# Kernel tuning notes

Measured on AMD Instinct MI355X. Metric: run time of the kernel, lower is better.

The kernel has to match this reference:

```python
import jax, jax.numpy as jnp
import numpy as np

B, S, H = 1, 2048, 2048
NH, NKV, HD = 16, 4, 128
F, E, TOPK = 4096, 8, 2
EPS = 1e-5
THETA = 10000.0
NEG = -1e30


def setup_inputs() -> dict:
    key = jax.random.key(0)
    ks = jax.random.split(key, 12)
    s = 0.02
    f32 = jnp.float32
    return {
        "positions": jnp.arange(S, dtype=jnp.int32),
        "hidden_states": jax.random.normal(ks[0], (B, S, H), f32),
        "wq": jax.random.normal(ks[1], (H, NH * HD), f32) * s,
        "wk": jax.random.normal(ks[2], (H, NKV * HD), f32) * s,
        "wv": jax.random.normal(ks[3], (H, NKV * HD), f32) * s,
        "wo": jax.random.normal(ks[4], (NH * HD, H), f32) * s,
        "w_gate": jax.random.normal(ks[5], (H, E), f32) * s,
        "w1": jax.random.normal(ks[6], (E, H, F), f32) * s,
        "w2": jax.random.normal(ks[7], (E, F, H), f32) * s,
        "w3": jax.random.normal(ks[8], (E, H, F), f32) * s,
        "ln_in": jnp.ones((H,), f32),
        "ln_post": jnp.ones((H,), f32),
    }


def rmsnorm(x, w):
    var = jnp.mean(jnp.square(x.astype(jnp.float32)), axis=-1, keepdims=True)
    return (x.astype(jnp.float32) * jax.lax.rsqrt(var + EPS)).astype(x.dtype) * w


def apply_rope(x, positions):
    # x: [B, S, n, HD], neox style (rotate halves)
    half = HD // 2
    inv_freq = 1.0 / (THETA ** (jnp.arange(half, dtype=jnp.float32) * 2.0 / HD))
    ang = positions.astype(jnp.float32)[:, None] * inv_freq  # [S, half]
    cos = jnp.cos(ang)[None, :, None, :]
    sin = jnp.sin(ang)[None, :, None, :]
    x1, x2 = jnp.split(x, 2, axis=-1)
    return jnp.concatenate([x1 * cos - x2 * sin, x2 * cos + x1 * sin], axis=-1).astype(x.dtype)


def decoder_layer(positions, x, wq, wk, wv, wo, w_gate, w1, w2, w3, ln_in, ln_post):
    # residual is None branch: residual = x; h = input_layernorm(x)
    residual = x
    h = rmsnorm(x, ln_in)
    # --- attention ---
    q = (h @ wq).reshape(B, S, NH, HD)
    k = (h @ wk).reshape(B, S, NKV, HD)
    v = (h @ wv).reshape(B, S, NKV, HD)
    q = apply_rope(q, positions)
    k = apply_rope(k, positions)
    rep = NH // NKV  # GQA: repeat kv heads
    k = jnp.repeat(k, rep, axis=2)
    v = jnp.repeat(v, rep, axis=2)
    scores = jnp.einsum("bqhd,bkhd->bhqk", q, k) * (HD ** -0.5)
    causal = jnp.tril(jnp.ones((S, S), bool))
    scores = jnp.where(causal[None, None], scores, NEG)
    attn = jax.nn.softmax(scores, axis=-1)
    o = jnp.einsum("bhqk,bkhd->bqhd", attn, v).reshape(B, S, NH * HD) @ wo
    # --- fused add + post-attention RMSNorm ---
    residual = o + residual
    h = rmsnorm(residual, ln_post)
    # --- MoE: dense all-expert compute, mask-weighted combine ---
    xt = h.reshape(-1, H)  # [T, H]
    logits = xt @ w_gate
    rw = jax.nn.softmax(logits.astype(jnp.float32), axis=-1)  # [T, E]
    w_top, idx = jax.lax.top_k(rw, TOPK)
    w_top = w_top / jnp.sum(w_top, axis=-1, keepdims=True)
    T = xt.shape[0]
    combine = jnp.zeros((T, E), jnp.float32).at[jnp.arange(T)[:, None], idx].add(w_top)
    a = jnp.einsum("th,ehf->etf", xt, w1)  # [E, T, F]
    g = jax.nn.silu(a) * jnp.einsum("th,ehf->etf", xt, w3)
    out = jnp.einsum("etf,efh->eth", g, w2)  # [E, T, H]
    moe = jnp.einsum("eth,te->th", out, combine.astype(xt.dtype))
    return moe.reshape(B, S, H), residual


def reference(positions, hidden_states, wq, wk, wv, wo, w_gate, w1, w2, w3, ln_in, ln_post):
    return decoder_layer(positions, hidden_states, wq, wk, wv, wo, w_gate, w1, w2, w3, ln_in, ln_post)
```

## Files before the change

kernel.cpp:

```cpp
#include <hip/hip_runtime.h>

typedef _Float16 f16x8 __attribute__((ext_vector_type(8)));
typedef _Float16 f16x2 __attribute__((ext_vector_type(2)));
typedef float f32x4 __attribute__((ext_vector_type(4)));

#define DEV __device__ __forceinline__

struct alignas(16) H8 { _Float16 h[8]; };
struct alignas(8)  H4 { _Float16 h[4]; };

DEV f32x4 mfma16(f16x8 a, f16x8 b, f32x4 c) {
  return __builtin_amdgcn_mfma_f32_16x16x32_f16(a, b, c, 0, 0, 0);
}

DEV f16x2 pkrtz(float a, float b) {
  return __builtin_bit_cast(f16x2, __builtin_amdgcn_cvt_pkrtz(a, b));
}

DEV H4 pack4(float a, float b, float c, float d) {
  union { f16x2 v[2]; H4 h; } u;
  u.v[0] = pkrtz(a, b);
  u.v[1] = pkrtz(c, d);
  return u.h;
}

DEV f16x8 frag_b36(const _Float16* b, int n, int kc) {
  const unsigned long long* p = (const unsigned long long*)(b + n*36 + kc*8);
  union { unsigned long long u[2]; f16x8 v; } r;
  r.u[0] = p[0]; r.u[1] = p[1];
  return r.v;
}

DEV float block_sum(float v, volatile float* red, int tid) {
  #pragma unroll
  for (int mm = 1; mm < 64; mm <<= 1) v += __shfl_xor(v, mm);
  if ((tid & 63) == 0) red[tid >> 6] = v;
  __syncthreads();
  return red[0] + red[1] + red[2] + red[3];
}

__global__ __launch_bounds__(256) void k_rmsnorm_split(
    const float* __restrict__ x, const float* __restrict__ w,
    _Float16* __restrict__ hi, _Float16* __restrict__ lo) {
  __shared__ float red[4];
  int row = blockIdx.x, tid = threadIdx.x;
  const float* xr = x + (size_t)row*2048 + tid*8;
  float xs[8];
  *(float4*)&xs[0] = *(const float4*)xr;
  *(float4*)&xs[4] = *(const float4*)(xr + 4);
  float ss = 0.f;
  #pragma unroll
  for (int j = 0; j < 8; ++j) ss += xs[j]*xs[j];
  float tot = block_sum(ss, red, tid);
  float sc = 1.0f / sqrtf(tot*(1.0f/2048.0f) + 1e-5f);
  const float* wr = w + tid*8;
  H8 ph, pl;
  #pragma unroll
  for (int j = 0; j < 8; ++j) {
    float o = xs[j]*sc*wr[j];
    _Float16 hh = (_Float16)o;
    ph.h[j] = hh; pl.h[j] = (_Float16)(o - (float)hh);
  }
  *(H8*)(hi + (size_t)row*2048 + tid*8) = ph;
  *(H8*)(lo + (size_t)row*2048 + tid*8) = pl;
}

template<bool RESID>
__global__ __launch_bounds__(256) void k_gemm(
    const _Float16* __restrict__ Ahi, const _Float16* __restrict__ Alo,
    const float* __restrict__ B, int N, int K,
    float* __restrict__ C,
    const float* __restrict__ resid_in, float* __restrict__ resid_out) {
  const int tid = threadIdx.x;
  const int l = tid & 63, w = tid >> 6;
  const int wm = w >> 1, wn = w & 1;
  const int row0 = blockIdx.y * 128, col0 = blockIdx.x * 128;

  __shared__ _Float16 aHi[128*32], aLo[128*32];
  __shared__ _Float16 bHi[128*36], bLo[128*36];

  f32x4 acc[4][4] = {};

  const int rS = tid >> 1, khalf = tid & 1;
  const int bn = tid & 127, bkg = tid >> 7;

  for (int k0 = 0; k0 < K; k0 += 32) {
    __syncthreads();
    {
      int c0 = khalf*2;
      int d0 = rS*32 + ((c0    ) ^ (rS&3))*8;
      int d1 = rS*32 + ((c0 + 1) ^ (rS&3))*8;
      const _Float16* ah = Ahi + (size_t)(row0 + rS)*K + k0 + khalf*16;
      const _Float16* al = Alo + (size_t)(row0 + rS)*K + k0 + khalf*16;
      *(H8*)&aHi[d0] = *(const H8*)ah;
      *(H8*)&aHi[d1] = *(const H8*)(ah + 8);
      *(H8*)&aLo[d0] = *(const H8*)al;
      *(H8*)&aLo[d1] = *(const H8*)(al + 8);
    }
    {
      const float* bp = B + (size_t)(k0 + bkg*16)*N + col0 + bn;
      float tv[16];
      #pragma unroll
      for (int i = 0; i < 16; ++i) tv[i] = bp[(size_t)i*N];
      #pragma unroll
      for (int q_ = 0; q_ < 4; ++q_) {
        H4 ph, pl;
        #pragma unroll
        for (int j = 0; j < 4; ++j) {
          float x = tv[q_*4 + j];
          _Float16 hh = (_Float16)x;
          ph.h[j] = hh; pl.h[j] = (_Float16)(x - (float)hh);
        }
        int ei = bn*36 + bkg*16 + q_*4;
        *(H4*)&bHi[ei] = ph;
        *(H4*)&bLo[ei] = pl;
      }
    }
    __syncthreads();
    {
      const int kc = l >> 4;
      f16x8 ah[4], al4[4];
      #pragma unroll
      for (int m = 0; m < 4; ++m) {
        int mr = wm*64 + m*16 + (l & 15);
        int cc = (kc ^ (mr & 3))*8;
        ah[m]  = *(const f16x8*)&aHi[mr*32 + cc];
        al4[m] = *(const f16x8*)&aLo[mr*32 + cc];
      }
      #pragma unroll
      for (int n = 0; n < 4; ++n) {
        int nr = wn*64 + n*16 + (l & 15);
        f16x8 bh = frag_b36(bHi, nr, kc);
        f16x8 bl = frag_b36(bLo, nr, kc);
        #pragma unroll
        for (int m = 0; m < 4; ++m) {
          acc[m][n] = mfma16(ah[m],  bh, acc[m][n]);
          acc[m][n] = mfma16(ah[m],  bl, acc[m][n]);
          acc[m][n] = mfma16(al4[m], bh, acc[m][n]);
        }
      }
    }
  }
  #pragma unroll
  for (int m = 0; m < 4; ++m)
    #pragma unroll
    for (int n = 0; n < 4; ++n)
      #pragma unroll
      for (int r = 0; r < 4; ++r) {
        int row = row0 + wm*64 + m*16 + (l>>4)*4 + r;
        int col = col0 + wn*64 + n*16 + (l&15);
        float v = acc[m][n][r];
        if constexpr (RESID) {
          size_t idx = (size_t)row*2048 + col;
          v += resid_in[idx];
          resid_out[idx] = v;
        } else {
          C[(size_t)row*N + col] = v;
        }
      }
}

__global__ __launch_bounds__(256) void k_rope(
    float* __restrict__ buf, const int* __restrict__ pos, int nh) {
  int s = blockIdx.x;
  int hh = blockIdx.y*4 + (threadIdx.x >> 6);
  int d = threadIdx.x & 63;
  float p = (float)pos[s];
  double ex = ((double)(2*d)/128.0) * 9.210340371976184;
  float pw = (float)exp(ex);
  float inv = 1.0f / pw;
  float ang = p * inv;
  float cs = cosf(ang), sn = sinf(ang);
  float* b = buf + (size_t)s*(nh*128) + hh*128 + d;
  float x1 = b[0], x2 = b[64];
  b[0]  = x1*cs - x2*sn;
  b[64] = x2*cs + x1*sn;
}

__global__ __launch_bounds__(256) void k_attn(
    const float* __restrict__ q, const float* __restrict__ k,
    const float* __restrict__ v,
    _Float16* __restrict__ o_hi, _Float16* __restrict__ o_lo) {
  const int qt = gridDim.x - 1 - blockIdx.x;
  const int h = blockIdx.y;
  const int tid = threadIdx.x, l = tid & 63, w = tid >> 6;
  const int qb = qt*64, qw = qb + w*16;
  const int kvh = h >> 2;

  __shared__ _Float16 kHi[32*128], kLo[32*128];
  __shared__ _Float16 vHi[128*32], vLo[128*32];
  __shared__ _Float16 pHi[4][16*40], pLo[4][16*40];

  f16x8 qh[4], ql[4];
  {
    int qrow = qw + (l & 15);
    const float* qp = q + (size_t)qrow*2048 + h*128 + (l>>4)*8;
    #pragma unroll
    for (int c = 0; c < 4; ++c)
      #pragma unroll
      for (int j = 0; j < 8; ++j) {
        float x = qp[c*32 + j];
        _Float16 hh = (_Float16)x;
        qh[c][j] = hh; ql[c][j] = (_Float16)(x - (float)hh);
      }
  }

  float mrun[4], lrun[4];
  f32x4 oacc[8] = {};
  #pragma unroll
  for (int r = 0; r < 4; ++r) { mrun[r] = -1e30f; lrun[r] = 0.f; }

  const int srow = tid >> 3, sc = (tid & 7)*2;

  for (int kv0 = 0; kv0 <= qb + 32; kv0 += 32) {
    __syncthreads();
    {
      const float* kp = k + (size_t)(kv0 + srow)*512 + kvh*128 + sc*8;
      const float* vp = v + (size_t)(kv0 + srow)*512 + kvh*128 + sc*8;
      #pragma unroll
      for (int cc = 0; cc < 2; ++cc) {
        int c = sc + cc;
        H8 ph, pl;
        #pragma unroll
        for (int j = 0; j < 8; ++j) {
          float x = kp[cc*8 + j];
          _Float16 hh = (_Float16)x;
          ph.h[j] = hh; pl.h[j] = (_Float16)(x - (float)hh);
        }
        int di = srow*128 + (c ^ (srow & 7))*8;
        *(H8*)&kHi[di] = ph;
        *(H8*)&kLo[di] = pl;
        #pragma unroll
        for (int j = 0; j < 8; ++j) {
          float x = vp[cc*8 + j];
          _Float16 hh = (_Float16)x;
          _Float16 ll = (_Float16)(x - (float)hh);
          int d = c*8 + j;
          int vi = d*32 + (((srow>>3) ^ (d&3)))*8 + (srow & 7);
          vHi[vi] = hh; vLo[vi] = ll;
        }
      }
    }
    __syncthreads();
    if (kv0 <= qw + 15) {
      f32x4 s[2] = {};
      #pragma unroll
      for (int nt = 0; nt < 2; ++nt) {
        int krow = nt*16 + (l & 15);
        #pragma unroll
        for (int c = 0; c < 4; ++c) {
          int ch = (c*4 + (l>>4)) ^ (krow & 7);
          f16x8 bh = *(const f16x8*)&kHi[krow*128 + ch*8];
          f16x8 bl = *(const f16x8*)&kLo[krow*128 + ch*8];
          s[nt] = mfma16(qh[c], bh, s[nt]);
          s[nt] = mfma16(qh[c], bl, s[nt]);
          s[nt] = mfma16(ql[c], bh, s[nt]);
        }
      }
      const float SC = 0.08838834764831845f;
      float sv[2][4];
      #pragma unroll
      for (int nt = 0; nt < 2; ++nt)
        #pragma unroll
        for (int r = 0; r < 4; ++r) {
          float val = s[nt][r]*SC;
          int qg = qw + (l>>4)*4 + r;
          int kg = kv0 + nt*16 + (l & 15);
          sv[nt][r] = (kg > qg) ? -1e30f : val;
        }
      float tm[4];
      #pragma unroll
      for (int r = 0; r < 4; ++r) tm[r] = fmaxf(sv[0][r], sv[1][r]);
      #pragma unroll
      for (int mm = 1; mm < 16; mm <<= 1)
        #pragma unroll
        for (int r = 0; r < 4; ++r) tm[r] = fmaxf(tm[r], __shfl_xor(tm[r], mm));
      float alpha[4], rs[4];
      #pragma unroll
      for (int r = 0; r < 4; ++r) {
        float mn = fmaxf(mrun[r], tm[r]);
        alpha[r] = expf(mrun[r] - mn);
        mrun[r] = mn;
      }
      float pv[2][4];
      #pragma unroll
      for (int nt = 0; nt < 2; ++nt)
        #pragma unroll
        for (int r = 0; r < 4; ++r) pv[nt][r] = expf(sv[nt][r] - mrun[r]);
      #pragma unroll
      for (int r = 0; r < 4; ++r) rs[r] = pv[0][r] + pv[1][r];
      #pragma unroll
      for (int mm = 1; mm < 16; mm <<= 1)
        #pragma unroll
        for (int r = 0; r < 4; ++r) rs[r] += __shfl_xor(rs[r], mm);
      #pragma unroll
      for (int r = 0; r < 4; ++r) lrun[r] = lrun[r]*alpha[r] + rs[r];
      #pragma unroll
      for (int dt = 0; dt < 8; ++dt)
        #pragma unroll
        for (int r = 0; r < 4; ++r) oacc[dt][r] *= alpha[r];
      #pragma unroll
      for (int nt = 0; nt < 2; ++nt)
        #pragma unroll
        for (int r = 0; r < 4; ++r) {
          float x = pv[nt][r];
          _Float16 hh = (_Float16)x;
          int qr = (l>>4)*4 + r, kc = nt*16 + (l & 15);
          pHi[w][qr*40 + kc] = hh;
          pLo[w][qr*40 + kc] = (_Float16)(x - (float)hh);
        }
      f16x8 pa = *(const f16x8*)&pHi[w][(l&15)*40 + (l>>4)*8];
      f16x8 pb = *(const f16x8*)&pLo[w][(l&15)*40 + (l>>4)*8];
      #pragma unroll
      for (int dt = 0; dt < 8; ++dt) {
        int d = dt*16 + (l & 15);
        int ch = ((l>>4) ^ (d & 3))*8;
        f16x8 vh = *(const f16x8*)&vHi[d*32 + ch];
        f16x8 vl = *(const f16x8*)&vLo[d*32 + ch];
        oacc[dt] = mfma16(pa, vh, oacc[dt]);
        oacc[dt] = mfma16(pa, vl, oacc[dt]);
        oacc[dt] = mfma16(pb, vh, oacc[dt]);
      }
    }
  }
  #pragma unroll
  for (int dt = 0; dt < 8; ++dt)
    #pragma unroll
    for (int r = 0; r < 4; ++r) {
      int qg = qw + (l>>4)*4 + r;
      float ov = oacc[dt][r] / lrun[r];
      _Float16 hh = (_Float16)ov;
      size_t idx = (size_t)qg*2048 + h*128 + dt*16 + (l&15);
      o_hi[idx] = hh;
      o_lo[idx] = (_Float16)(ov - (float)hh);
    }
}

__global__ __launch_bounds__(256) void k_postnorm_gate(
    const float* __restrict__ resid, const float* __restrict__ wln,
    const float* __restrict__ wg, _Float16* __restrict__ h2,
    float* __restrict__ logits) {
  __shared__ float red[4];
  __shared__ float red2[4][8];
  int row = blockIdx.x, tid = threadIdx.x;
  const float* xr = resid + (size_t)row*2048 + tid*8;
  float xs[8];
  *(float4*)&xs[0] = *(const float4*)xr;
  *(float4*)&xs[4] = *(const float4*)(xr + 4);
  float ss = 0.f;
  #pragma unroll
  for (int j = 0; j < 8; ++j) ss += xs[j]*xs[j];
  float tot = block_sum(ss, red, tid);
  float sc = 1.0f/sqrtf(tot*(1.0f/2048.0f) + 1e-5f);
  const float* wr = wln + tid*8;
  float hv[8];
  H8 ph;
  #pragma unroll
  for (int j = 0; j < 8; ++j) {
    hv[j] = xs[j]*sc*wr[j];
    ph.h[j] = (_Float16)hv[j];
  }
  *(H8*)(h2 + (size_t)row*2048 + tid*8) = ph;
  float lg[8] = {0,0,0,0,0,0,0,0};
  const float* wgp = wg + (size_t)tid*8*8;
  #pragma unroll
  for (int j = 0; j < 8; ++j)
    #pragma unroll
    for (int e = 0; e < 8; ++e) lg[e] += hv[j]*wgp[j*8 + e];
  #pragma unroll
  for (int mm = 1; mm < 64; mm <<= 1)
    #pragma unroll
    for (int e = 0; e < 8; ++e) lg[e] += __shfl_xor(lg[e], mm);
  if ((tid & 63) == 0)
    #pragma unroll
    for (int e = 0; e < 8; ++e) red2[tid>>6][e] = lg[e];
  __syncthreads();
  if (tid < 8)
    logits[(size_t)row*8 + tid] = red2[0][tid]+red2[1][tid]+red2[2][tid]+red2[3][tid];
}

__global__ __launch_bounds__(256) void k_route(
    const float* __restrict__ logits, int* __restrict__ counts,
    int* __restrict__ slot_tok, float* __restrict__ slot_w) {
  int t = blockIdx.x*256 + threadIdx.x;
  if (t >= 2048) return;
  float lg[8];
  #pragma unroll
  for (int e = 0; e < 8; ++e) lg[e] = logits[t*8 + e];
  int a = 0; float la = lg[0];
  #pragma unroll
  for (int e = 1; e < 8; ++e) if (lg[e] > la) { la = lg[e]; a = e; }
  int b = -1; float lb = -3e38f;
  #pragma unroll
  for (int e = 0; e < 8; ++e) if (e != a && lg[e] > lb) { lb = lg[e]; b = e; }
  float wa = 1.f/(1.f + expf(lb - la));
  float wb = 1.f - wa;
  int sa = atomicAdd(&counts[a], 1);
  slot_tok[a*2048 + sa] = t; slot_w[a*2048 + sa] = wa;
  int sb = atomicAdd(&counts[b], 1);
  slot_tok[b*2048 + sb] = t; slot_w[b*2048 + sb] = wb;
}

__global__ void k_scan(const int* __restrict__ counts, int* __restrict__ offs) {
  if (threadIdx.x == 0) {
    int o_ = 0;
    #pragma unroll
    for (int e = 0; e < 8; ++e) { offs[e] = o_; o_ += counts[e]; }
  }
}

__global__ __launch_bounds__(256) void k_moe1(
    const _Float16* __restrict__ h2, const float* __restrict__ w1,
    const float* __restrict__ w3, const int* __restrict__ counts,
    const int* __restrict__ offs, const int* __restrict__ slot_tok,
    _Float16* __restrict__ g) {
  int bid = blockIdx.x;
  int e = bid >> 10, mt = (bid >> 6) & 15, nt = bid & 63;
  int cnt = counts[e];
  if (mt*128 >= cnt) return;
  const int tid = threadIdx.x, l = tid & 63, w = tid >> 6;
  const int wm = w >> 1, wn = w & 1;
  __shared__ _Float16 aT[128*32];
  __shared__ _Float16 b1[64*36], b3[64*36];
  const int rS = tid >> 1, khalf = tid & 1;
  int slot = mt*128 + rS;
  int tok = (slot < cnt) ? slot_tok[e*2048 + slot] : slot_tok[e*2048];
  const _Float16* arow = h2 + (size_t)tok*2048;
  const float* w1e = w1 + (size_t)e*2048*4096;
  const float* w3e = w3 + (size_t)e*2048*4096;
  const int bn = tid & 63, bkg = tid >> 6;
  f32x4 acc1[4][2] = {}, acc3[4][2] = {};
  for (int k0 = 0; k0 < 2048; k0 += 32) {
    __syncthreads();
    {
      const _Float16* ap = arow + k0 + khalf*16;
      int c0 = khalf*2;
      *(H8*)&aT[rS*32 + ((c0  )^(rS&3))*8] = *(const H8*)ap;
      *(H8*)&aT[rS*32 + ((c0+1)^(rS&3))*8] = *(const H8*)(ap + 8);
    }
    {
      const float* bp1 = w1e + (size_t)(k0 + bkg*8)*4096 + nt*64 + bn;
      const float* bp3 = w3e + (size_t)(k0 + bkg*8)*4096 + nt*64 + bn;
      float t1[8], t3[8];
      #pragma unroll
      for (int i = 0; i < 8; ++i) { t1[i] = bp1[(size_t)i*4096]; t3[i] = bp3[(size_t)i*4096]; }
      int ei = bn*36 + bkg*8;
      *(H4*)&b1[ei]     = pack4(t1[0], t1[1], t1[2], t1[3]);
      *(H4*)&b1[ei + 4] = pack4(t1[4], t1[5], t1[6], t1[7]);
      *(H4*)&b3[ei]     = pack4(t3[0], t3[1], t3[2], t3[3]);
      *(H4*)&b3[ei + 4] = pack4(t3[4], t3[5], t3[6], t3[7]);
    }
    __syncthreads();
    {
      const int kc = l >> 4;
      f16x8 a_[4];
      #pragma unroll
      for (int m = 0; m < 4; ++m) {
        int mr = wm*64 + m*16 + (l & 15);
        a_[m] = *(const f16x8*)&aT[mr*32 + (kc ^ (mr&3))*8];
      }
      #pragma unroll
      for (int n = 0; n < 2; ++n) {
        int nr = wn*32 + n*16 + (l & 15);
        f16x8 bb1 = frag_b36(b1, nr, kc);
        f16x8 bb3 = frag_b36(b3, nr, kc);
        #pragma unroll
        for (int m = 0; m < 4; ++m) {
          acc1[m][n] = mfma16(a_[m], bb1, acc1[m][n]);
          acc3[m][n] = mfma16(a_[m], bb3, acc3[m][n]);
        }
      }
    }
  }
  int ge = offs[e];
  #pragma unroll
  for (int m = 0; m < 4; ++m)
    #pragma unroll
    for (int n = 0; n < 2; ++n)
      #pragma unroll
      for (int r = 0; r < 4; ++r) {
        int srow2 = mt*128 + wm*64 + m*16 + (l>>4)*4 + r;
        if (srow2 < cnt) {
          float x1 = acc1[m][n][r], x3 = acc3[m][n][r];
          float gg = (x1/(1.f + expf(-x1)))*x3;
          int col = nt*64 + wn*32 + n*16 + (l&15);
          g[(size_t)(ge + srow2)*4096 + col] = (_Float16)gg;
        }
      }
}

__global__ __launch_bounds__(256) void k_moe2(
    const _Float16* __restrict__ g, const float* __restrict__ w2,
    const int* __restrict__ counts, const int* __restrict__ offs,
    const int* __restrict__ slot_tok, const float* __restrict__ slot_w,
    float* __restrict__ out) {
  int bid = blockIdx.x;
  int e = bid >> 8, mt = (bid >> 4) & 15, nt = bid & 15;
  int cnt = counts[e];
  if (mt*128 >= cnt) return;
  const int tid = threadIdx.x, l = tid & 63, w = tid >> 6;
  const int wm = w >> 1, wn = w & 1;
  __shared__ _Float16 aT[128*32];
  __shared__ _Float16 bT[128*36];
  const int rS = tid >> 1, khalf = tid & 1;
  int ge = offs[e];
  int slot = mt*128 + rS;
  const _Float16* arow = g + (size_t)(ge + (slot < cnt ? slot : 0))*4096;
  const float* w2e = w2 + (size_t)e*4096*2048;
  const int bn = tid & 127, bkg = tid >> 7;
  f32x4 acc[4][4] = {};
  for (int k0 = 0; k0 < 4096; k0 += 32) {
    __syncthreads();
    {
      const _Float16* ap = arow + k0 + khalf*16;
      int c0 = khalf*2;
      *(H8*)&aT[rS*32 + ((c0  )^(rS&3))*8] = *(const H8*)ap;
      *(H8*)&aT[rS*32 + ((c0+1)^(rS&3))*8] = *(const H8*)(ap + 8);
    }
    {
      const float* bp = w2e + (size_t)(k0 + bkg*16)*2048 + nt*128 + bn;
      float tv[16];
      #pragma unroll
      for (int i = 0; i < 16; ++i) tv[i] = bp[(size_t)i*2048];
      int ei = bn*36 + bkg*16;
      *(H4*)&bT[ei]      = pack4(tv[0],  tv[1],  tv[2],  tv[3]);
      *(H4*)&bT[ei + 4]  = pack4(tv[4],  tv[5],  tv[6],  tv[7]);
      *(H4*)&bT[ei + 8]  = pack4(tv[8],  tv[9],  tv[10], tv[11]);
      *(H4*)&bT[ei + 12] = pack4(tv[12], tv[13], tv[14], tv[15]);
    }
    __syncthreads();
    {
      const int kc = l >> 4;
      f16x8 a_[4];
      #pragma unroll
      for (int m = 0; m < 4; ++m) {
        int mr = wm*64 + m*16 + (l&15);
        a_[m] = *(const f16x8*)&aT[mr*32 + (kc ^ (mr&3))*8];
      }
      #pragma unroll
      for (int n = 0; n < 4; ++n) {
        f16x8 bb = frag_b36(bT, wn*64 + n*16 + (l&15), kc);
        #pragma unroll
        for (int m = 0; m < 4; ++m) acc[m][n] = mfma16(a_[m], bb, acc[m][n]);
      }
    }
  }
  #pragma unroll
  for (int m = 0; m < 4; ++m)
    #pragma unroll
    for (int r = 0; r < 4; ++r) {
      int srow2 = mt*128 + wm*64 + m*16 + (l>>4)*4 + r;
      if (srow2 < cnt) {
        int tok = slot_tok[e*2048 + srow2];
        float wt = slot_w[e*2048 + srow2];
        #pragma unroll
        for (int n = 0; n < 4; ++n) {
          int col = nt*128 + wn*64 + n*16 + (l&15);
          atomicAdd(&out[(size_t)tok*2048 + col], wt*acc[m][n][r]);
        }
      }
    }
}

extern "C" void kernel_launch(void* const* d_in, const int* in_sizes, int n_in,
                              void* d_out, int out_size, void* d_ws, size_t ws_size,
                              hipStream_t stream) {
  const int*   positions = (const int*)d_in[0];
  const float* x   = (const float*)d_in[1];
  const float* wq  = (const float*)d_in[2];
  const float* wk  = (const float*)d_in[3];
  const float* wv  = (const float*)d_in[4];
  const float* wo  = (const float*)d_in[5];
  const float* wg  = (const float*)d_in[6];
  const float* w1  = (const float*)d_in[7];
  const float* w2  = (const float*)d_in[8];
  const float* w3  = (const float*)d_in[9];
  const float* ln_in   = (const float*)d_in[10];
  const float* ln_post = (const float*)d_in[11];

  float* moe_out   = (float*)d_out;
  float* resid_out = (float*)d_out + (size_t)4194304;

  char* ws = (char*)d_ws;
  _Float16* h_hi   = (_Float16*)(ws);
  _Float16* h_lo   = (_Float16*)(ws + 8388608);
  float*    qbuf   = (float*)(ws + 16777216);
  float*    kbuf   = (float*)(ws + 33554432);
  float*    vbuf   = (float*)(ws + 37748736);
  _Float16* o_hi   = (_Float16*)(ws + 41943040);
  _Float16* o_lo   = (_Float16*)(ws + 50331648);
  _Float16* h2     = (_Float16*)(ws + 58720256);
  float*    logits = (float*)(ws + 67108864);
  int*      counts = (int*)(ws + 67174400);
  int*      offs   = (int*)(ws + 67174656);
  int*      slot_tok = (int*)(ws + 67174912);
  float*    slot_w   = (float*)(ws + 67240448);
  _Float16* gbuf   = (_Float16*)ws;

  hipMemsetAsync(moe_out, 0, (size_t)4194304*4, stream);
  hipMemsetAsync(counts, 0, 32, stream);

  k_rmsnorm_split<<<2048, 256, 0, stream>>>(x, ln_in, h_hi, h_lo);
  k_gemm<false><<<dim3(16,16), 256, 0, stream>>>(h_hi, h_lo, wq, 2048, 2048, qbuf, nullptr, nullptr);
  k_gemm<false><<<dim3(4,16),  256, 0, stream>>>(h_hi, h_lo, wk,  512, 2048, kbuf, nullptr, nullptr);
  k_gemm<false><<<dim3(4,16),  256, 0, stream>>>(h_hi, h_lo, wv,  512, 2048, vbuf, nullptr, nullptr);
  k_rope<<<dim3(2048,4), 256, 0, stream>>>(qbuf, positions, 16);
  k_rope<<<dim3(2048,1), 256, 0, stream>>>(kbuf, positions, 4);
  k_attn<<<dim3(32,16), 256, 0, stream>>>(qbuf, kbuf, vbuf, o_hi, o_lo);
  k_gemm<true><<<dim3(16,16), 256, 0, stream>>>(o_hi, o_lo, wo, 2048, 2048, nullptr, x, resid_out);
  k_postnorm_gate<<<2048, 256, 0, stream>>>(resid_out, ln_post, wg, h2, logits);
  k_route<<<8, 256, 0, stream>>>(logits, counts, slot_tok, slot_w);
  k_scan<<<1, 64, 0, stream>>>(counts, offs);
  k_moe1<<<8192, 256, 0, stream>>>(h2, w1, w3, counts, offs, slot_tok, gbuf);
  k_moe2<<<2048, 256, 0, stream>>>(gbuf, w2, counts, offs, slot_tok, slot_w, moe_out);
}
```

Measured before the change: 1.300 ms.

## Double MoE GEMM K-tile to 64 and vectorize fp16 split conversions

The MoE expert GEMMs (moe1 and moe2) now stage 64-wide K tiles instead of 32. That halves the number of barrier pairs per output tile, and B fragments are read as aligned 128-bit LDS loads from a 72-element padded row. The fp32-to-fp16 hi/lo split used by the dense GEMM and attention is rewritten with packed cvt_pkrtz conversions and float4 global loads. The larger tiles raise LDS use per block, which may lower occupancy. The switch to round-toward-zero conversion slightly changes the rounding of the hi/lo split.

```diff
diff --git a/kernel.cpp b/kernel.cpp
--- a/kernel.cpp
+++ b/kernel.cpp
@@ -9,6 +9,8 @@
 struct alignas(16) H8 { _Float16 h[8]; };
 struct alignas(8)  H4 { _Float16 h[4]; };
 
+union U8 { f16x2 v[4]; f16x8 x; H8 h; };
+
 DEV f32x4 mfma16(f16x8 a, f16x8 b, f32x4 c) {
   return __builtin_amdgcn_mfma_f32_16x16x32_f16(a, b, c, 0, 0, 0);
 }
@@ -17,11 +19,24 @@
   return __builtin_bit_cast(f16x2, __builtin_amdgcn_cvt_pkrtz(a, b));
 }
 
-DEV H4 pack4(float a, float b, float c, float d) {
-  union { f16x2 v[2]; H4 h; } u;
-  u.v[0] = pkrtz(a, b);
-  u.v[1] = pkrtz(c, d);
+DEV H8 cvt8(const float* t) {
+  U8 u;
+  #pragma unroll
+  for (int j = 0; j < 4; ++j) u.v[j] = pkrtz(t[2*j], t[2*j+1]);
   return u.h;
+}
+
+DEV void split8v(const float* t, f16x8& hi, f16x8& lo) {
+  U8 H_, L_;
+  #pragma unroll
+  for (int j = 0; j < 4; ++j) {
+    f16x2 hh = pkrtz(t[2*j], t[2*j+1]);
+    float r0 = t[2*j]   - (float)hh[0];
+    float r1 = t[2*j+1] - (float)hh[1];
+    H_.v[j] = hh;
+    L_.v[j] = pkrtz(r0, r1);
+  }
+  hi = H_.x; lo = L_.x;
 }
 
 DEV f16x8 frag_b36(const _Float16* b, int n, int kc) {
@@ -102,19 +117,15 @@
       float tv[16];
       #pragma unroll
       for (int i = 0; i < 16; ++i) tv[i] = bp[(size_t)i*N];
-      #pragma unroll
-      for (int q_ = 0; q_ < 4; ++q_) {
-        H4 ph, pl;
-        #pragma unroll
-        for (int j = 0; j < 4; ++j) {
-          float x = tv[q_*4 + j];
-          _Float16 hh = (_Float16)x;
-          ph.h[j] = hh; pl.h[j] = (_Float16)(x - (float)hh);
-        }
-        int ei = bn*36 + bkg*16 + q_*4;
-        *(H4*)&bHi[ei] = ph;
-        *(H4*)&bLo[ei] = pl;
-      }
+      f16x8 h0, l0, h1, l1;
+      split8v(tv, h0, l0);
+      split8v(tv + 8, h1, l1);
+      int ei = bn*36 + bkg*16;
+      const H4* hp;
+      hp = (const H4*)&h0; *(H4*)&bHi[ei]      = hp[0]; *(H4*)&bHi[ei + 4]  = hp[1];
+      hp = (const H4*)&h1; *(H4*)&bHi[ei + 8]  = hp[0]; *(H4*)&bHi[ei + 12] = hp[1];
+      hp = (const H4*)&l0; *(H4*)&bLo[ei]      = hp[0]; *(H4*)&bLo[ei + 4]  = hp[1];
+      hp = (const H4*)&l1; *(H4*)&bLo[ei + 8]  = hp[0]; *(H4*)&bLo[ei + 12] = hp[1];
     }
     __syncthreads();
     {
@@ -196,13 +207,12 @@
     int qrow = qw + (l & 15);
     const float* qp = q + (size_t)qrow*2048 + h*128 + (l>>4)*8;
     #pragma unroll
-    for (int c = 0; c < 4; ++c)
-      #pragma unroll
-      for (int j = 0; j < 8; ++j) {
-        float x = qp[c*32 + j];
-        _Float16 hh = (_Float16)x;
-        qh[c][j] = hh; ql[c][j] = (_Float16)(x - (float)hh);
-      }
+    for (int c = 0; c < 4; ++c) {
+      float t[8];
+      *(float4*)&t[0] = *(const float4*)(qp + c*32);
+      *(float4*)&t[4] = *(const float4*)(qp + c*32 + 4);
+      split8v(t, qh[c], ql[c]);
+    }
   }
 
   float mrun[4], lrun[4];
@@ -220,19 +230,20 @@
       #pragma unroll
       for (int cc = 0; cc < 2; ++cc) {
         int c = sc + cc;
-        H8 ph, pl;
+        float tk[8];
+        *(float4*)&tk[0] = *(const float4*)(kp + cc*8);
+        *(float4*)&tk[4] = *(const float4*)(kp + cc*8 + 4);
+        f16x8 hx, lx;
+        split8v(tk, hx, lx);
+        int di = srow*128 + (c ^ (srow & 7))*8;
+        *(H8*)&kHi[di] = *(const H8*)&hx;
+        *(H8*)&kLo[di] = *(const H8*)&lx;
+        float tv_[8];
+        *(float4*)&tv_[0] = *(const float4*)(vp + cc*8);
+        *(float4*)&tv_[4] = *(const float4*)(vp + cc*8 + 4);
         #pragma unroll
         for (int j = 0; j < 8; ++j) {
-          float x = kp[cc*8 + j];
-          _Float16 hh = (_Float16)x;
-          ph.h[j] = hh; pl.h[j] = (_Float16)(x - (float)hh);
-        }
-        int di = srow*128 + (c ^ (srow & 7))*8;
-        *(H8*)&kHi[di] = ph;
-        *(H8*)&kLo[di] = pl;
-        #pragma unroll
-        for (int j = 0; j < 8; ++j) {
-          float x = vp[cc*8 + j];
+          float x = tv_[j];
           _Float16 hh = (_Float16)x;
           _Float16 ll = (_Float16)(x - (float)hh);
           int d = c*8 + j;
@@ -420,8 +431,8 @@
   if (mt*128 >= cnt) return;
   const int tid = threadIdx.x, l = tid & 63, w = tid >> 6;
   const int wm = w >> 1, wn = w & 1;
-  __shared__ _Float16 aT[128*32];
-  __shared__ _Float16 b1[64*36], b3[64*36];
+  __shared__ _Float16 aT[128*64];
+  __shared__ _Float16 b1[64*72], b3[64*72];
   const int rS = tid >> 1, khalf = tid & 1;
   int slot = mt*128 + rS;
   int tok = (slot < cnt) ? slot_tok[e*2048 + slot] : slot_tok[e*2048];
@@ -430,40 +441,45 @@
   const float* w3e = w3 + (size_t)e*2048*4096;
   const int bn = tid & 63, bkg = tid >> 6;
   f32x4 acc1[4][2] = {}, acc3[4][2] = {};
-  for (int k0 = 0; k0 < 2048; k0 += 32) {
-    __syncthreads();
-    {
-      const _Float16* ap = arow + k0 + khalf*16;
-      int c0 = khalf*2;
-      *(H8*)&aT[rS*32 + ((c0  )^(rS&3))*8] = *(const H8*)ap;
-      *(H8*)&aT[rS*32 + ((c0+1)^(rS&3))*8] = *(const H8*)(ap + 8);
-    }
-    {
-      const float* bp1 = w1e + (size_t)(k0 + bkg*8)*4096 + nt*64 + bn;
-      const float* bp3 = w3e + (size_t)(k0 + bkg*8)*4096 + nt*64 + bn;
-      float t1[8], t3[8];
-      #pragma unroll
-      for (int i = 0; i < 8; ++i) { t1[i] = bp1[(size_t)i*4096]; t3[i] = bp3[(size_t)i*4096]; }
-      int ei = bn*36 + bkg*8;
-      *(H4*)&b1[ei]     = pack4(t1[0], t1[1], t1[2], t1[3]);
-      *(H4*)&b1[ei + 4] = pack4(t1[4], t1[5], t1[6], t1[7]);
-      *(H4*)&b3[ei]     = pack4(t3[0], t3[1], t3[2], t3[3]);
-      *(H4*)&b3[ei + 4] = pack4(t3[4], t3[5], t3[6], t3[7]);
-    }
-    __syncthreads();
-    {
-      const int kc = l >> 4;
+  for (int k0 = 0; k0 < 2048; k0 += 64) {
+    __syncthreads();
+    {
+      const _Float16* ap = arow + k0 + khalf*32;
+      #pragma unroll
+      for (int c = 0; c < 4; ++c) {
+        int cc = khalf*4 + c;
+        *(H8*)&aT[rS*64 + ((cc ^ (rS&7))*8)] = *(const H8*)(ap + c*8);
+      }
+    }
+    {
+      #pragma unroll
+      for (int s = 0; s < 2; ++s) {
+        const float* p1 = w1e + (size_t)(k0 + bkg*16 + s*8)*4096 + nt*64 + bn;
+        float t[8];
+        #pragma unroll
+        for (int i = 0; i < 8; ++i) t[i] = p1[(size_t)i*4096];
+        *(H8*)&b1[bn*72 + bkg*16 + s*8] = cvt8(t);
+        const float* p3 = w3e + (size_t)(k0 + bkg*16 + s*8)*4096 + nt*64 + bn;
+        #pragma unroll
+        for (int i = 0; i < 8; ++i) t[i] = p3[(size_t)i*4096];
+        *(H8*)&b3[bn*72 + bkg*16 + s*8] = cvt8(t);
+      }
+    }
+    __syncthreads();
+    #pragma unroll
+    for (int kk2 = 0; kk2 < 2; ++kk2) {
+      const int kc = kk2*4 + (l >> 4);
       f16x8 a_[4];
       #pragma unroll
       for (int m = 0; m < 4; ++m) {
         int mr = wm*64 + m*16 + (l & 15);
-        a_[m] = *(const f16x8*)&aT[mr*32 + (kc ^ (mr&3))*8];
+        a_[m] = *(const f16x8*)&aT[mr*64 + ((kc ^ (mr&7))*8)];
       }
       #pragma unroll
       for (int n = 0; n < 2; ++n) {
         int nr = wn*32 + n*16 + (l & 15);
-        f16x8 bb1 = frag_b36(b1, nr, kc);
-        f16x8 bb3 = frag_b36(b3, nr, kc);
+        f16x8 bb1 = *(const f16x8*)&b1[nr*72 + kc*8];
+        f16x8 bb3 = *(const f16x8*)&b3[nr*72 + kc*8];
         #pragma unroll
         for (int m = 0; m < 4; ++m) {
           acc1[m][n] = mfma16(a_[m], bb1, acc1[m][n]);
@@ -500,8 +516,8 @@
   if (mt*128 >= cnt) return;
   const int tid = threadIdx.x, l = tid & 63, w = tid >> 6;
   const int wm = w >> 1, wn = w & 1;
-  __shared__ _Float16 aT[128*32];
-  __shared__ _Float16 bT[128*36];
+  __shared__ _Float16 aT[128*64];
+  __shared__ _Float16 bT[128*72];
   const int rS = tid >> 1, khalf = tid & 1;
   int ge = offs[e];
   int slot = mt*128 + rS;
@@ -509,37 +525,40 @@
   const float* w2e = w2 + (size_t)e*4096*2048;
   const int bn = tid & 127, bkg = tid >> 7;
   f32x4 acc[4][4] = {};
-  for (int k0 = 0; k0 < 4096; k0 += 32) {
-    __syncthreads();
-    {
-      const _Float16* ap = arow + k0 + khalf*16;
-      int c0 = khalf*2;
-      *(H8*)&aT[rS*32 + ((c0  )^(rS&3))*8] = *(const H8*)ap;
-      *(H8*)&aT[rS*32 + ((c0+1)^(rS&3))*8] = *(const H8*)(ap + 8);
-    }
-    {
-      const float* bp = w2e + (size_t)(k0 + bkg*16)*2048 + nt*128 + bn;
-      float tv[16];
-      #pragma unroll
-      for (int i = 0; i < 16; ++i) tv[i] = bp[(size_t)i*2048];
-      int ei = bn*36 + bkg*16;
-      *(H4*)&bT[ei]      = pack4(tv[0],  tv[1],  tv[2],  tv[3]);
-      *(H4*)&bT[ei + 4]  = pack4(tv[4],  tv[5],  tv[6],  tv[7]);
-      *(H4*)&bT[ei + 8]  = pack4(tv[8],  tv[9],  tv[10], tv[11]);
-      *(H4*)&bT[ei + 12] = pack4(tv[12], tv[13], tv[14], tv[15]);
-    }
-    __syncthreads();
-    {
-      const int kc = l >> 4;
+  for (int k0 = 0; k0 < 4096; k0 += 64) {
+    __syncthreads();
+    {
+      const _Float16* ap = arow + k0 + khalf*32;
+      #pragma unroll
+      for (int c = 0; c < 4; ++c) {
+        int cc = khalf*4 + c;
+        *(H8*)&aT[rS*64 + ((cc ^ (rS&7))*8)] = *(const H8*)(ap + c*8);
+      }
+    }
+    {
+      #pragma unroll
+      for (int s = 0; s < 4; ++s) {
+        const float* p = w2e + (size_t)(k0 + bkg*32 + s*8)*2048 + nt*128 + bn;
+        float t[8];
+        #pragma unroll
+        for (int i = 0; i < 8; ++i) t[i] = p[(size_t)i*2048];
+        *(H8*)&bT[bn*72 + bkg*32 + s*8] = cvt8(t);
+      }
+    }
+    __syncthreads();
+    #pragma unroll
+    for (int kk2 = 0; kk2 < 2; ++kk2) {
+      const int kc = kk2*4 + (l >> 4);
       f16x8 a_[4];
       #pragma unroll
       for (int m = 0; m < 4; ++m) {
-        int mr = wm*64 + m*16 + (l&15);
-        a_[m] = *(const f16x8*)&aT[mr*32 + (kc ^ (mr&3))*8];
+        int mr = wm*64 + m*16 + (l & 15);
+        a_[m] = *(const f16x8*)&aT[mr*64 + ((kc ^ (mr&7))*8)];
       }
       #pragma unroll
       for (int n = 0; n < 4; ++n) {
-        f16x8 bb = frag_b36(bT, wn*64 + n*16 + (l&15), kc);
+        int nr = wn*64 + n*16 + (l & 15);
+        f16x8 bb = *(const f16x8*)&bT[nr*72 + kc*8];
         #pragma unroll
         for (int m = 0; m < 4; ++m) acc[m][n] = mfma16(a_[m], bb, acc[m][n]);
       }
```

New measurement: 1.335 ms. 1.03x slower.

## Split-K the projection GEMMs with atomic accumulation and vectorize fp16 hi/lo splitting

Applied to the files above, without the earlier changes.

Converts the Q/K/V/O projection GEMMs to split-K kernels that accumulate into pre-zeroed (or residual-prefilled) outputs with float atomicAdd. This raises the block count on the small K/V GEMMs and the 256-block Q/O GEMMs so more compute units stay busy. The residual add moves into a device memcpy of x into the output before the O-projection. The change also vectorizes the fp16 hi/lo split using packed conversions and float4 loads in the GEMM B loader and attention Q/K loads. The cost is extra memsets and a copy, atomic traffic, and a summation order that is no longer deterministic.

```diff
diff --git a/kernel.cpp b/kernel.cpp
--- a/kernel.cpp
+++ b/kernel.cpp
@@ -8,6 +8,8 @@
 
 struct alignas(16) H8 { _Float16 h[8]; };
 struct alignas(8)  H4 { _Float16 h[4]; };
+
+union U8 { f16x2 v[4]; f16x8 x; H8 h; };
 
 DEV f32x4 mfma16(f16x8 a, f16x8 b, f32x4 c) {
   return __builtin_amdgcn_mfma_f32_16x16x32_f16(a, b, c, 0, 0, 0);
@@ -22,6 +24,19 @@
   u.v[0] = pkrtz(a, b);
   u.v[1] = pkrtz(c, d);
   return u.h;
+}
+
+DEV void split8v(const float* t, f16x8& hi, f16x8& lo) {
+  U8 H_, L_;
+  #pragma unroll
+  for (int j = 0; j < 4; ++j) {
+    f16x2 hh = pkrtz(t[2*j], t[2*j+1]);
+    float r0 = t[2*j]   - (float)hh[0];
+    float r1 = t[2*j+1] - (float)hh[1];
+    H_.v[j] = hh;
+    L_.v[j] = pkrtz(r0, r1);
+  }
+  hi = H_.x; lo = L_.x;
 }
 
 DEV f16x8 frag_b36(const _Float16* b, int n, int kc) {
@@ -65,16 +80,16 @@
   *(H8*)(lo + (size_t)row*2048 + tid*8) = pl;
 }
 
-template<bool RESID>
-__global__ __launch_bounds__(256) void k_gemm(
+__global__ __launch_bounds__(256) void k_gemm_ks(
     const _Float16* __restrict__ Ahi, const _Float16* __restrict__ Alo,
     const float* __restrict__ B, int N, int K,
-    float* __restrict__ C,
-    const float* __restrict__ resid_in, float* __restrict__ resid_out) {
+    float* __restrict__ C) {
   const int tid = threadIdx.x;
   const int l = tid & 63, w = tid >> 6;
   const int wm = w >> 1, wn = w & 1;
   const int row0 = blockIdx.y * 128, col0 = blockIdx.x * 128;
+  const int kz = K / gridDim.z;
+  const int kbase = blockIdx.z * kz;
 
   __shared__ _Float16 aHi[128*32], aLo[128*32];
   __shared__ _Float16 bHi[128*36], bLo[128*36];
@@ -84,7 +99,7 @@
   const int rS = tid >> 1, khalf = tid & 1;
   const int bn = tid & 127, bkg = tid >> 7;
 
-  for (int k0 = 0; k0 < K; k0 += 32) {
+  for (int k0 = kbase; k0 < kbase + kz; k0 += 32) {
     __syncthreads();
     {
       int c0 = khalf*2;
@@ -102,19 +117,15 @@
       float tv[16];
       #pragma unroll
       for (int i = 0; i < 16; ++i) tv[i] = bp[(size_t)i*N];
-      #pragma unroll
-      for (int q_ = 0; q_ < 4; ++q_) {
-        H4 ph, pl;
-        #pragma unroll
-        for (int j = 0; j < 4; ++j) {
-          float x = tv[q_*4 + j];
-          _Float16 hh = (_Float16)x;
-          ph.h[j] = hh; pl.h[j] = (_Float16)(x - (float)hh);
-        }
-        int ei = bn*36 + bkg*16 + q_*4;
-        *(H4*)&bHi[ei] = ph;
-        *(H4*)&bLo[ei] = pl;
-      }
+      f16x8 h0, l0, h1, l1;
+      split8v(tv, h0, l0);
+      split8v(tv + 8, h1, l1);
+      int ei = bn*36 + bkg*16;
+      const H4* hp;
+      hp = (const H4*)&h0; *(H4*)&bHi[ei]      = hp[0]; *(H4*)&bHi[ei + 4]  = hp[1];
+      hp = (const H4*)&h1; *(H4*)&bHi[ei + 8]  = hp[0]; *(H4*)&bHi[ei + 12] = hp[1];
+      hp = (const H4*)&l0; *(H4*)&bLo[ei]      = hp[0]; *(H4*)&bLo[ei + 4]  = hp[1];
+      hp = (const H4*)&l1; *(H4*)&bLo[ei + 8]  = hp[0]; *(H4*)&bLo[ei + 12] = hp[1];
     }
     __syncthreads();
     {
@@ -149,14 +160,7 @@
       for (int r = 0; r < 4; ++r) {
         int row = row0 + wm*64 + m*16 + (l>>4)*4 + r;
         int col = col0 + wn*64 + n*16 + (l&15);
-        float v = acc[m][n][r];
-        if constexpr (RESID) {
-          size_t idx = (size_t)row*2048 + col;
-          v += resid_in[idx];
-          resid_out[idx] = v;
-        } else {
-          C[(size_t)row*N + col] = v;
-        }
+        atomicAdd(&C[(size_t)row*N + col], acc[m][n][r]);
       }
 }
 
@@ -196,13 +200,12 @@
     int qrow = qw + (l & 15);
     const float* qp = q + (size_t)qrow*2048 + h*128 + (l>>4)*8;
     #pragma unroll
-    for (int c = 0; c < 4; ++c)
-      #pragma unroll
-      for (int j = 0; j < 8; ++j) {
-        float x = qp[c*32 + j];
-        _Float16 hh = (_Float16)x;
-        qh[c][j] = hh; ql[c][j] = (_Float16)(x - (float)hh);
-      }
+    for (int c = 0; c < 4; ++c) {
+      float t[8];
+      *(float4*)&t[0] = *(const float4*)(qp + c*32);
+      *(float4*)&t[4] = *(const float4*)(qp + c*32 + 4);
+      split8v(t, qh[c], ql[c]);
+    }
   }
 
   float mrun[4], lrun[4];
@@ -220,19 +223,20 @@
       #pragma unroll
       for (int cc = 0; cc < 2; ++cc) {
         int c = sc + cc;
-        H8 ph, pl;
+        float tk[8];
+        *(float4*)&tk[0] = *(const float4*)(kp + cc*8);
+        *(float4*)&tk[4] = *(const float4*)(kp + cc*8 + 4);
+        f16x8 hx, lx;
+        split8v(tk, hx, lx);
+        int di = srow*128 + (c ^ (srow & 7))*8;
+        *(H8*)&kHi[di] = *(const H8*)&hx;
+        *(H8*)&kLo[di] = *(const H8*)&lx;
+        float tv_[8];
+        *(float4*)&tv_[0] = *(const float4*)(vp + cc*8);
+        *(float4*)&tv_[4] = *(const float4*)(vp + cc*8 + 4);
         #pragma unroll
         for (int j = 0; j < 8; ++j) {
-          float x = kp[cc*8 + j];
-          _Float16 hh = (_Float16)x;
-          ph.h[j] = hh; pl.h[j] = (_Float16)(x - (float)hh);
-        }
-        int di = srow*128 + (c ^ (srow & 7))*8;
-        *(H8*)&kHi[di] = ph;
-        *(H8*)&kLo[di] = pl;
-        #pragma unroll
-        for (int j = 0; j < 8; ++j) {
-          float x = vp[cc*8 + j];
+          float x = tv_[j];
           _Float16 hh = (_Float16)x;
           _Float16 ll = (_Float16)(x - (float)hh);
           int d = c*8 + j;
@@ -597,17 +601,21 @@
   float*    slot_w   = (float*)(ws + 67240448);
   _Float16* gbuf   = (_Float16*)ws;
 
+  hipMemsetAsync(qbuf, 0, 16777216, stream);
+  hipMemsetAsync(kbuf, 0, 4194304, stream);
+  hipMemsetAsync(vbuf, 0, 4194304, stream);
+  hipMemcpyAsync(resid_out, x, (size_t)4194304*4, hipMemcpyDeviceToDevice, stream);
   hipMemsetAsync(moe_out, 0, (size_t)4194304*4, stream);
   hipMemsetAsync(counts, 0, 32, stream);
 
   k_rmsnorm_split<<<2048, 256, 0, stream>>>(x, ln_in, h_hi, h_lo);
-  k_gemm<false><<<dim3(16,16), 256, 0, stream>>>(h_hi, h_lo, wq, 2048, 2048, qbuf, nullptr, nullptr);
-  k_gemm<false><<<dim3(4,16),  256, 0, stream>>>(h_hi, h_lo, wk,  512, 2048, kbuf, nullptr, nullptr);
-  k_gemm<false><<<dim3(4,16),  256, 0, stream>>>(h_hi, h_lo, wv,  512, 2048, vbuf, nullptr, nullptr);
+  k_gemm_ks<<<dim3(16,16,2), 256, 0, stream>>>(h_hi, h_lo, wq, 2048, 2048, qbuf);
+  k_gemm_ks<<<dim3(4,16,4),  256, 0, stream>>>(h_hi, h_lo, wk,  512, 2048, kbuf);
+  k_gemm_ks<<<dim3(4,16,4),  256, 0, stream>>>(h_hi, h_lo, wv,  512, 2048, vbuf);
   k_rope<<<dim3(2048,4), 256, 0, stream>>>(qbuf, positions, 16);
   k_rope<<<dim3(2048,1), 256, 0, stream>>>(kbuf, positions, 4);
   k_attn<<<dim3(32,16), 256, 0, stream>>>(qbuf, kbuf, vbuf, o_hi, o_lo);
-  k_gemm<true><<<dim3(16,16), 256, 0, stream>>>(o_hi, o_lo, wo, 2048, 2048, nullptr, x, resid_out);
+  k_gemm_ks<<<dim3(16,16,2), 256, 0, stream>>>(o_hi, o_lo, wo, 2048, 2048, resid_out);
   k_postnorm_gate<<<2048, 256, 0, stream>>>(resid_out, ln_post, wg, h2, logits);
   k_route<<<8, 256, 0, stream>>>(logits, counts, slot_tok, slot_w);
   k_scan<<<1, 64, 0, stream>>>(counts, offs);
```

New measurement: 1.135 ms. 1.15x faster.
